# Kernel tuning notes

Hardware: AMD Instinct MI355X
Metric: run time of the kernel (lower is better)

## Reference

```python
import jax, jax.numpy as jnp
import numpy as np

B, S, D = 1, 2048, 2048
HQ, HKV = 32, 8
HD = D // HQ            # 64
G = HQ // HKV           # 4 query heads per kv head


def setup_inputs() -> dict:
    key = jax.random.key(0)
    ks = jax.random.split(key, 5)
    x = jax.random.normal(ks[0], (B, S, D), jnp.float32)
    # RoPE tables (theta = 10000), shape [S, HD//2]
    inv_freq = 1.0 / (10000.0 ** (np.arange(0, HD, 2, dtype=np.float64) / HD))
    angles = np.outer(np.arange(S, dtype=np.float64), inv_freq)
    freqs_cos = jnp.asarray(np.cos(angles), jnp.float32)
    freqs_sin = jnp.asarray(np.sin(angles), jnp.float32)
    # additive causal mask [1,1,S,S]: 0 on/below diagonal, large negative above
    i = jnp.arange(S)
    causal_mask = jnp.where(i[None, :] <= i[:, None], 0.0, -1e9).astype(jnp.float32)[None, None]
    sc = 1.0 / np.sqrt(D)
    Wq = jax.random.normal(ks[1], (D, HQ * HD), jnp.float32) * sc
    Wk = jax.random.normal(ks[2], (D, HKV * HD), jnp.float32) * sc
    Wv = jax.random.normal(ks[3], (D, HKV * HD), jnp.float32) * sc
    Wo = jax.random.normal(ks[4], (D, D), jnp.float32) * sc
    return {"x": x, "freqs_cos": freqs_cos, "freqs_sin": freqs_sin,
            "causal_mask": causal_mask, "Wq": Wq, "Wk": Wk, "Wv": Wv, "Wo": Wo}


def _rope(t, cos, sin):
    # t: [B,S,H,HD]; complex multiply on interleaved (even, odd) pairs
    b, s, h, d = t.shape
    t2 = t.reshape(b, s, h, d // 2, 2)
    t0, t1 = t2[..., 0], t2[..., 1]
    c = cos[None, :, None, :]
    sn = sin[None, :, None, :]
    out = jnp.stack([t0 * c - t1 * sn, t0 * sn + t1 * c], axis=-1)
    return out.reshape(b, s, h, d)


def reference(x, freqs_cos, freqs_sin, causal_mask, Wq, Wk, Wv, Wo):
    b, s, _ = x.shape
    q = (x @ Wq).reshape(b, s, HQ, HD)
    k = (x @ Wk).reshape(b, s, HKV, HD)
    v = (x @ Wv).reshape(b, s, HKV, HD)
    q = _rope(q, freqs_cos, freqs_sin)
    k = _rope(k, freqs_cos, freqs_sin)
    # GQA without materializing repeat_kv: group query heads per kv head
    q = q.transpose(0, 2, 1, 3).reshape(b, HKV, G, s, HD)   # [b,kv,g,s,d]
    k = k.transpose(0, 2, 1, 3)                              # [b,kv,s,d]
    v = v.transpose(0, 2, 1, 3)                              # [b,kv,s,d]
    scores = jnp.einsum('bkgsd,bktd->bkgst', q, k) / jnp.sqrt(jnp.float32(HD))
    scores = scores + causal_mask[:, :, None]                # [1,1,1,S,S] broadcast
    probs = jax.nn.softmax(scores, axis=-1)
    out = jnp.einsum('bkgst,bktd->bkgsd', probs, v)          # [b,kv,g,s,d]
    out = out.transpose(0, 3, 1, 2, 4).reshape(b, s, D)      # merge heads in (kv,g) order
    return out @ Wo
```

## Files before the change

kernel.cpp:

```cpp
#include <hip/hip_runtime.h>

#define SEQ 2048
#define DMODEL 2048

typedef __attribute__((ext_vector_type(8))) _Float16 half8;
typedef __attribute__((ext_vector_type(4))) float f32x4;
typedef __attribute__((ext_vector_type(16))) float f32x16;

typedef const __attribute__((address_space(1))) void* gptr_t;
typedef __attribute__((address_space(3))) void* lptr_t;

static __device__ __forceinline__ void gload16(const void* g, void* l) {
  __builtin_amdgcn_global_load_lds((gptr_t)g, (lptr_t)l, 16, 0, 0);
}

static __device__ __forceinline__ unsigned short f2h(float f) {
  _Float16 h = (_Float16)f;
  union { _Float16 h; unsigned short u; } v; v.h = h;
  return v.u;
}

static __device__ __forceinline__ unsigned int pkh2(float a, float b) {
  union { __fp16 __attribute__((ext_vector_type(2))) h; unsigned int u; } v;
  v.h = __builtin_amdgcn_cvt_pkrtz(a, b);
  return v.u;
}

__global__ void k_cvt(const float* __restrict__ in, unsigned short* __restrict__ out, int n) {
  int i = (blockIdx.x * 256 + threadIdx.x) * 4;
  if (i >= n) return;
  float4 v = *(const float4*)(in + i);
  ushort4 o;
  o.x = f2h(v.x); o.y = f2h(v.y); o.z = f2h(v.z); o.w = f2h(v.w);
  *(ushort4*)(out + i) = o;
}

__global__ void k_tcvt(const float* __restrict__ in, unsigned short* __restrict__ out,
                       int K, int N, int ldin) {
  __shared__ float tile[32][33];
  int n0 = blockIdx.x * 32, k0 = blockIdx.y * 32;
  int tx = threadIdx.x, ty = threadIdx.y;
  #pragma unroll
  for (int j = ty; j < 32; j += 8)
    tile[j][tx] = in[(long)(k0 + j) * ldin + n0 + tx];
  __syncthreads();
  #pragma unroll
  for (int j = ty; j < 32; j += 8)
    out[(long)(n0 + j) * K + k0 + tx] = f2h(tile[tx][j]);
}

__global__ void k_tvp(const unsigned short* __restrict__ in, unsigned short* __restrict__ out) {
  __shared__ unsigned short tile[32][33];
  int c0 = blockIdx.x * 32, s0 = blockIdx.y * 32;
  int tx = threadIdx.x, ty = threadIdx.y;
  #pragma unroll
  for (int j = ty; j < 32; j += 8)
    tile[j][tx] = in[(long)(s0 + j) * 512 + c0 + tx];
  __syncthreads();
  #pragma unroll
  for (int j = ty; j < 32; j += 8) {
    int c = c0 + j;
    int s = s0 + tx;
    int sp = (s & ~12) | ((s & 8) >> 1) | ((s & 4) << 1);
    out[((long)(c >> 6) * 64 + (c & 63)) * SEQ + sp] = tile[tx][j];
  }
}

static __device__ __forceinline__ bool gemm_core(const unsigned short* __restrict__ A,
                                                 const unsigned short* __restrict__ B,
                                                 int K, char* SM, long m0, long n0,
                                                 int& wmO, int& wnO, f32x4 acc[4][4]) {
  int t = threadIdx.x;
  int l = t & 63, w = t >> 6;
  int ks = w & 1, wm = (w >> 2) & 1, wn = (w >> 1) & 1;
  int lr = l & 15, lh = l >> 4;
  wmO = wm; wnO = wn;
  unsigned short* As = (unsigned short*)SM;
  unsigned short* Bs = (unsigned short*)(SM + 32768);

  const unsigned short* Ag = A + (m0 + (t >> 3)) * K + (((t & 7) ^ ((t >> 3) & 7)) * 8);
  const unsigned short* Bg = B + (n0 + (t >> 3)) * K + (((t & 7) ^ ((t >> 3) & 7)) * 8);

  #pragma unroll
  for (int i = 0; i < 4; i++)
    #pragma unroll
    for (int j = 0; j < 4; j++)
      acc[i][j] = (f32x4){0.f, 0.f, 0.f, 0.f};

#define STG(buf, k0) do { \
    gload16(Ag + (k0), As + (buf) * 8192 + t * 8); \
    gload16(Ag + 64 * K + (k0), As + (buf) * 8192 + 4096 + t * 8); \
    gload16(Bg + (k0), Bs + (buf) * 8192 + t * 8); \
    gload16(Bg + 64 * K + (k0), Bs + (buf) * 8192 + 4096 + t * 8); \
  } while (0)

  int T = K >> 6;
  STG(0, 0);
  asm volatile("s_waitcnt vmcnt(0)" ::: "memory");
  __builtin_amdgcn_s_barrier();

  for (int ph = 0; ph < T; ph++) {
    if (ph + 1 < T) STG((ph + 1) & 1, (ph + 1) * 64);
    const unsigned short* Ab = As + (ph & 1) * 8192;
    const unsigned short* Bb = Bs + (ph & 1) * 8192;
    half8 a[4], b[4];
    #pragma unroll
    for (int mf = 0; mf < 4; mf++) {
      int ra = wm * 64 + mf * 16 + lr;
      a[mf] = *(const half8*)&Ab[ra * 64 + (((ks * 4 + lh) ^ (ra & 7)) * 8)];
    }
    #pragma unroll
    for (int nf = 0; nf < 4; nf++) {
      int rb = wn * 64 + nf * 16 + lr;
      b[nf] = *(const half8*)&Bb[rb * 64 + (((ks * 4 + lh) ^ (rb & 7)) * 8)];
    }
    #pragma unroll
    for (int mf = 0; mf < 4; mf++)
      #pragma unroll
      for (int nf = 0; nf < 4; nf++)
        acc[mf][nf] = __builtin_amdgcn_mfma_f32_16x16x32_f16(a[mf], b[nf], acc[mf][nf], 0, 0, 0);
    asm volatile("s_waitcnt vmcnt(0)" ::: "memory");
    __builtin_amdgcn_s_barrier();
  }
#undef STG

  __syncthreads();
  float* red = (float*)SM;
  int p = wm * 2 + wn;
  if (ks == 1) {
    #pragma unroll
    for (int mf = 0; mf < 4; mf++)
      #pragma unroll
      for (int nf = 0; nf < 4; nf++)
        *(f32x4*)&red[p * 4096 + l * 64 + (((mf * 4 + nf) ^ (l & 15)) << 2)] = acc[mf][nf];
  }
  __syncthreads();
  if (ks == 0) {
    #pragma unroll
    for (int mf = 0; mf < 4; mf++)
      #pragma unroll
      for (int nf = 0; nf < 4; nf++)
        acc[mf][nf] += *(const f32x4*)&red[p * 4096 + l * 64 + (((mf * 4 + nf) ^ (l & 15)) << 2)];
  }
  return ks == 0;
}

__global__ __launch_bounds__(512) void k_gemm(const unsigned short* __restrict__ A,
                                              const unsigned short* __restrict__ B,
                                              float* __restrict__ C, int M, int N, int K) {
  __shared__ __align__(16) char SM[65536];
  int l = threadIdx.x & 63;
  int lr = l & 15, lh = l >> 4;
  long m0 = (long)blockIdx.y * 128, n0 = (long)blockIdx.x * 128;
  f32x4 acc[4][4];
  int wm, wn;
  bool own = gemm_core(A, B, K, SM, m0, n0, wm, wn, acc);
  if (own) {
    #pragma unroll
    for (int mf = 0; mf < 4; mf++)
      #pragma unroll
      for (int nf = 0; nf < 4; nf++)
        #pragma unroll
        for (int i = 0; i < 4; i++)
          C[(m0 + wm * 64 + mf * 16 + lh * 4 + i) * N + n0 + wn * 64 + nf * 16 + lr] = acc[mf][nf][i];
  }
}

__global__ __launch_bounds__(512) void k_gemm_qkv(const unsigned short* __restrict__ A,
                                                  const unsigned short* __restrict__ B,
                                                  unsigned short* __restrict__ Qr,
                                                  unsigned short* __restrict__ Kr,
                                                  unsigned short* __restrict__ Vr,
                                                  const float* __restrict__ fc,
                                                  const float* __restrict__ fs, int K) {
  __shared__ __align__(16) char SM[65536];
  int l = threadIdx.x & 63;
  int lr = l & 15, lh = l >> 4;
  long m0 = (long)blockIdx.y * 128, n0 = (long)blockIdx.x * 128;
  f32x4 acc[4][4];
  int wm, wn;
  bool own = gemm_core(A, B, K, SM, m0, n0, wm, wn, acc);
  if (!own) return;

  const float SC = 0.125f * 1.44269504f;
  int n0i = (int)n0;
  if (n0i < 2560) {
    bool isQ = n0i < 2048;
    float scl = isQ ? SC : 1.0f;
    #pragma unroll
    for (int mf = 0; mf < 4; mf++)
      #pragma unroll
      for (int i = 0; i < 4; i++) {
        int row = (int)m0 + wm * 64 + mf * 16 + lh * 4 + i;
        const float* fcr = fc + row * 32;
        const float* fsr = fs + row * 32;
        #pragma unroll
        for (int nf = 0; nf < 4; nf++) {
          float v = acc[mf][nf][i];
          float pv = __shfl_xor(v, 1);
          int col = n0i + wn * 64 + nf * 16 + lr;
          int j = (col & 63) >> 1;
          float c_ = fcr[j] * scl, s_ = fsr[j] * scl;
          float o = (lr & 1) ? (pv * s_ + v * c_) : (v * c_ - pv * s_);
          if (isQ) Qr[(long)row * 2048 + col] = f2h(o);
          else {
            int cc = col - 2048;
            Kr[((long)(cc >> 6) * SEQ + row) * 64 + (cc & 63)] = f2h(o);
          }
        }
      }
  } else {
    #pragma unroll
    for (int mf = 0; mf < 4; mf++)
      #pragma unroll
      for (int i = 0; i < 4; i++) {
        int row = (int)m0 + wm * 64 + mf * 16 + lh * 4 + i;
        #pragma unroll
        for (int nf = 0; nf < 4; nf++) {
          int col = n0i + wn * 64 + nf * 16 + lr;
          Vr[(long)row * 512 + (col - 2560)] = f2h(acc[mf][nf][i]);
        }
      }
  }
}

__global__ __launch_bounds__(256) void k_attn(const unsigned short* __restrict__ Qr,
                                              const unsigned short* __restrict__ Kr,
                                              const unsigned short* __restrict__ Vg,
                                              unsigned short* __restrict__ AO) {
  __shared__ unsigned short KT[2][8192];
  __shared__ unsigned short VT[2][8192];
  __shared__ float gbuf[4][32];

  int tt = threadIdx.x;
  int wid = tt >> 6, l = tt & 63;
  int q = l & 31, hs = l >> 5;
  int h = blockIdx.x, hkv = h >> 2;
  int by = (int)gridDim.y - 1 - blockIdx.y;
  int dt = 4 * by + wid;
  int q0 = by * 128 + wid * 32;

  const unsigned short* Kh = Kr + (long)hkv * SEQ * 64;
  const unsigned short* Vh = Vg + (long)hkv * 64 * SEQ;

  int skr = tt >> 3, skc = tt & 7;
  int svr = tt >> 2, svc = tt & 3;
  const unsigned short* Ksrc = Kh + (long)skr * 64 + ((skc * 8) ^ ((skr & 7) << 3));
  const unsigned short* Vsrc = Vh + (long)svr * SEQ + ((svc * 8) ^ ((svr & 3) << 3));

#define ASTAGE(si) do { \
    int buf_ = (si) & 1; \
    _Pragma("unroll") for (int sub_ = 0; sub_ < 4; sub_++) { \
      int t0_ = ((si) * 4 + sub_) * 32; \
      gload16(Ksrc + (long)t0_ * 64, &KT[buf_][sub_ * 2048 + tt * 8]); \
      gload16(Vsrc + t0_, &VT[buf_][sub_ * 2048 + tt * 8]); \
    } \
  } while (0)

  half8 Qf[4];
  #pragma unroll
  for (int d = 0; d < 4; d++)
    Qf[d] = *(const half8*)&Qr[(long)(q0 + q) * 2048 + h * 64 + d * 16 + 8 * hs];

  f32x16 O0, O1;
  #pragma unroll
  for (int r = 0; r < 16; r++) { O0[r] = 0.f; O1[r] = 0.f; }
  float lsum = 0.f;

  ASTAGE(0);
  asm volatile("s_waitcnt vmcnt(0)" ::: "memory");
  __builtin_amdgcn_s_barrier();

  for (int si = 0; si <= by; si++) {
    if (si + 1 <= by) ASTAGE(si + 1);

    int buf = si & 1;
    #pragma unroll
    for (int sub = 0; sub < 4; sub++) {
      int ti = si * 4 + sub;
      if (ti <= dt) {
        const unsigned short* Ks = &KT[buf][sub * 2048];
        const unsigned short* Vs = &VT[buf][sub * 2048];
        half8 Kf[4], Vf[2][2];
        #pragma unroll
        for (int d = 0; d < 4; d++) {
          int e0 = d * 16 + 8 * hs;
          Kf[d] = *(const half8*)&Ks[q * 64 + (e0 ^ ((q & 7) << 3))];
        }
        #pragma unroll
        for (int ks = 0; ks < 2; ks++)
          #pragma unroll
          for (int nf = 0; nf < 2; nf++) {
            int d = q + 32 * nf;
            int e0 = ks * 16 + 8 * hs;
            Vf[ks][nf] = *(const half8*)&Vs[d * 32 + (e0 ^ ((d & 3) << 3))];
          }

        f32x16 S;
        #pragma unroll
        for (int r = 0; r < 16; r++) S[r] = 0.f;
        #pragma unroll
        for (int d = 0; d < 4; d++)
          S = __builtin_amdgcn_mfma_f32_32x32x16_f16(Kf[d], Qf[d], S, 0, 0, 0);

        bool dg = (ti == dt);
        float p[16];
        #pragma unroll
        for (int r = 0; r < 16; r++) {
          float v = S[r];
          if (dg) {
            int key = (r & 3) + 8 * (r >> 2) + 4 * hs;
            if (key > q) v = -1e30f;
          }
          p[r] = __builtin_exp2f(v - 8.0f);
          lsum += p[r];
        }

        union { unsigned int u[4]; half8 hh; } f0, f1;
        #pragma unroll
        for (int c = 0; c < 4; c++) {
          f0.u[c] = pkh2(p[2 * c], p[2 * c + 1]);
          f1.u[c] = pkh2(p[8 + 2 * c], p[9 + 2 * c]);
        }

        O0 = __builtin_amdgcn_mfma_f32_32x32x16_f16(f0.hh, Vf[0][0], O0, 0, 0, 0);
        O0 = __builtin_amdgcn_mfma_f32_32x32x16_f16(f1.hh, Vf[1][0], O0, 0, 0, 0);
        O1 = __builtin_amdgcn_mfma_f32_32x32x16_f16(f0.hh, Vf[0][1], O1, 0, 0, 0);
        O1 = __builtin_amdgcn_mfma_f32_32x32x16_f16(f1.hh, Vf[1][1], O1, 0, 0, 0);
      }
    }

    asm volatile("s_waitcnt vmcnt(0)" ::: "memory");
    __builtin_amdgcn_s_barrier();
  }
#undef ASTAGE

  lsum += __shfl_xor(lsum, 32);
  if (l < 32) gbuf[wid][l] = 1.f / lsum;
  asm volatile("" ::: "memory");
  #pragma unroll
  for (int r = 0; r < 16; r++) {
    int row = (r & 3) + 8 * (r >> 2) + 4 * hs;
    float ri = gbuf[wid][row];
    AO[(long)(q0 + row) * 2048 + h * 64 + q] = f2h(O0[r] * ri);
    AO[(long)(q0 + row) * 2048 + h * 64 + q + 32] = f2h(O1[r] * ri);
  }
}

extern "C" void kernel_launch(void* const* d_in, const int* in_sizes, int n_in,
                              void* d_out, int out_size, void* d_ws, size_t ws_size,
                              hipStream_t stream) {
  const float* x  = (const float*)d_in[0];
  const float* fc = (const float*)d_in[1];
  const float* fs = (const float*)d_in[2];
  const float* Wq = (const float*)d_in[4];
  const float* Wk = (const float*)d_in[5];
  const float* Wv = (const float*)d_in[6];
  const float* Wo = (const float*)d_in[7];
  float* out = (float*)d_out;

  char* ws = (char*)d_ws;
  unsigned short* xb  = (unsigned short*)(ws);
  unsigned short* WT  = (unsigned short*)(ws + (8l  << 20));
  unsigned short* WoT = (unsigned short*)(ws + (20l << 20));
  unsigned short* Qr  = (unsigned short*)(ws + (28l << 20));
  unsigned short* Kr  = (unsigned short*)(ws + (36l << 20));
  unsigned short* Vr  = (unsigned short*)(ws + (38l << 20));
  unsigned short* Vt  = (unsigned short*)(ws + (40l << 20));
  unsigned short* AO  = xb;

  dim3 tb(32, 8);
  k_cvt<<<4096, 256, 0, stream>>>(x, xb, 2048 * 2048);
  k_tcvt<<<dim3(64, 64), tb, 0, stream>>>(Wq, WT, 2048, 2048, 2048);
  k_tcvt<<<dim3(16, 64), tb, 0, stream>>>(Wk, WT + 2048l * 2048, 2048, 512, 512);
  k_tcvt<<<dim3(16, 64), tb, 0, stream>>>(Wv, WT + 2560l * 2048, 2048, 512, 512);
  k_tcvt<<<dim3(64, 64), tb, 0, stream>>>(Wo, WoT, 2048, 2048, 2048);

  k_gemm_qkv<<<dim3(24, 16), 512, 0, stream>>>(xb, WT, Qr, Kr, Vr, fc, fs, 2048);

  k_tvp<<<dim3(16, 64), tb, 0, stream>>>(Vr, Vt);

  k_attn<<<dim3(32, 16), 256, 0, stream>>>(Qr, Kr, Vt, AO);

  k_gemm<<<dim3(16, 16), 512, 0, stream>>>(AO, WoT, out, 2048, 2048, 2048);
}
```

Measured before the change: 156.9 us.

## Re-layout V tiles in LDS and specialize diagonal masking in attention loop

Changes the V staging layout in shared memory so each lane reads contiguous 8-element chunks indexed by (kslice, d), replacing the XOR-swizzled layout, and changes the global-to-LDS load mapping to match. Splits the per-subtile loop into a templated tile function with separate masked and unmasked variants. Full stages now run four unmasked tiles with no per-tile branch, and the diagonal stage runs only the needed tiles before one masked tile. The aim is to cut LDS bank conflicts and branch/select overhead in the inner loop. The cost is more code and possibly different global load coalescing for V.

```diff
diff --git a/kernel.cpp b/kernel.cpp
--- a/kernel.cpp
+++ b/kernel.cpp
@@ -224,6 +224,55 @@
   }
 }
 
+template <bool DG>
+static __device__ __forceinline__ void attn_tile(const unsigned short* __restrict__ Ks,
+                                                 const unsigned short* __restrict__ Vs,
+                                                 int q, int hs, const half8 (&Qf)[4],
+                                                 f32x16& O0, f32x16& O1, float& lsum) {
+  half8 Kf[4], Vf[2][2];
+  #pragma unroll
+  for (int d = 0; d < 4; d++) {
+    int e0 = d * 16 + 8 * hs;
+    Kf[d] = *(const half8*)&Ks[q * 64 + (e0 ^ ((q & 7) << 3))];
+  }
+  #pragma unroll
+  for (int ks = 0; ks < 2; ks++)
+    #pragma unroll
+    for (int nf = 0; nf < 2; nf++)
+      Vf[ks][nf] = *(const half8*)&Vs[(2 * ks + hs) * 512 + (q + 32 * nf) * 8];
+
+  f32x16 S;
+  #pragma unroll
+  for (int r = 0; r < 16; r++) S[r] = 0.f;
+  #pragma unroll
+  for (int d = 0; d < 4; d++)
+    S = __builtin_amdgcn_mfma_f32_32x32x16_f16(Kf[d], Qf[d], S, 0, 0, 0);
+
+  float p[16];
+  #pragma unroll
+  for (int r = 0; r < 16; r++) {
+    float v = S[r];
+    if (DG) {
+      int key = (r & 3) + 8 * (r >> 2) + 4 * hs;
+      if (key > q) v = -1e30f;
+    }
+    p[r] = __builtin_exp2f(v - 8.0f);
+    lsum += p[r];
+  }
+
+  union { unsigned int u[4]; half8 hh; } f0, f1;
+  #pragma unroll
+  for (int c = 0; c < 4; c++) {
+    f0.u[c] = pkh2(p[2 * c], p[2 * c + 1]);
+    f1.u[c] = pkh2(p[8 + 2 * c], p[9 + 2 * c]);
+  }
+
+  O0 = __builtin_amdgcn_mfma_f32_32x32x16_f16(f0.hh, Vf[0][0], O0, 0, 0, 0);
+  O0 = __builtin_amdgcn_mfma_f32_32x32x16_f16(f1.hh, Vf[1][0], O0, 0, 0, 0);
+  O1 = __builtin_amdgcn_mfma_f32_32x32x16_f16(f0.hh, Vf[0][1], O1, 0, 0, 0);
+  O1 = __builtin_amdgcn_mfma_f32_32x32x16_f16(f1.hh, Vf[1][1], O1, 0, 0, 0);
+}
+
 __global__ __launch_bounds__(256) void k_attn(const unsigned short* __restrict__ Qr,
                                               const unsigned short* __restrict__ Kr,
                                               const unsigned short* __restrict__ Vg,
@@ -244,9 +293,8 @@
   const unsigned short* Vh = Vg + (long)hkv * 64 * SEQ;
 
   int skr = tt >> 3, skc = tt & 7;
-  int svr = tt >> 2, svc = tt & 3;
   const unsigned short* Ksrc = Kh + (long)skr * 64 + ((skc * 8) ^ ((skr & 7) << 3));
-  const unsigned short* Vsrc = Vh + (long)svr * SEQ + ((svc * 8) ^ ((svr & 3) << 3));
+  const unsigned short* Vsrc = Vh + (long)(tt & 63) * SEQ + ((tt >> 6) * 8);
 
 #define ASTAGE(si) do { \
     int buf_ = (si) & 1; \
@@ -275,59 +323,18 @@
     if (si + 1 <= by) ASTAGE(si + 1);
 
     int buf = si & 1;
-    #pragma unroll
-    for (int sub = 0; sub < 4; sub++) {
-      int ti = si * 4 + sub;
-      if (ti <= dt) {
-        const unsigned short* Ks = &KT[buf][sub * 2048];
-        const unsigned short* Vs = &VT[buf][sub * 2048];
-        half8 Kf[4], Vf[2][2];
-        #pragma unroll
-        for (int d = 0; d < 4; d++) {
-          int e0 = d * 16 + 8 * hs;
-          Kf[d] = *(const half8*)&Ks[q * 64 + (e0 ^ ((q & 7) << 3))];
-        }
-        #pragma unroll
-        for (int ks = 0; ks < 2; ks++)
-          #pragma unroll
-          for (int nf = 0; nf < 2; nf++) {
-            int d = q + 32 * nf;
-            int e0 = ks * 16 + 8 * hs;
-            Vf[ks][nf] = *(const half8*)&Vs[d * 32 + (e0 ^ ((d & 3) << 3))];
-          }
-
-        f32x16 S;
-        #pragma unroll
-        for (int r = 0; r < 16; r++) S[r] = 0.f;
-        #pragma unroll
-        for (int d = 0; d < 4; d++)
-          S = __builtin_amdgcn_mfma_f32_32x32x16_f16(Kf[d], Qf[d], S, 0, 0, 0);
-
-        bool dg = (ti == dt);
-        float p[16];
-        #pragma unroll
-        for (int r = 0; r < 16; r++) {
-          float v = S[r];
-          if (dg) {
-            int key = (r & 3) + 8 * (r >> 2) + 4 * hs;
-            if (key > q) v = -1e30f;
-          }
-          p[r] = __builtin_exp2f(v - 8.0f);
-          lsum += p[r];
-        }
-
-        union { unsigned int u[4]; half8 hh; } f0, f1;
-        #pragma unroll
-        for (int c = 0; c < 4; c++) {
-          f0.u[c] = pkh2(p[2 * c], p[2 * c + 1]);
-          f1.u[c] = pkh2(p[8 + 2 * c], p[9 + 2 * c]);
-        }
-
-        O0 = __builtin_amdgcn_mfma_f32_32x32x16_f16(f0.hh, Vf[0][0], O0, 0, 0, 0);
-        O0 = __builtin_amdgcn_mfma_f32_32x32x16_f16(f1.hh, Vf[1][0], O0, 0, 0, 0);
-        O1 = __builtin_amdgcn_mfma_f32_32x32x16_f16(f0.hh, Vf[0][1], O1, 0, 0, 0);
-        O1 = __builtin_amdgcn_mfma_f32_32x32x16_f16(f1.hh, Vf[1][1], O1, 0, 0, 0);
-      }
+    const unsigned short* Kb = &KT[buf][0];
+    const unsigned short* Vb = &VT[buf][0];
+    int rem = dt - si * 4 + 1;
+    if (rem > 4) {
+      attn_tile<false>(Kb, Vb, q, hs, Qf, O0, O1, lsum);
+      attn_tile<false>(Kb + 2048, Vb + 2048, q, hs, Qf, O0, O1, lsum);
+      attn_tile<false>(Kb + 4096, Vb + 4096, q, hs, Qf, O0, O1, lsum);
+      attn_tile<false>(Kb + 6144, Vb + 6144, q, hs, Qf, O0, O1, lsum);
+    } else if (rem > 0) {
+      for (int sub = 0; sub < rem - 1; sub++)
+        attn_tile<false>(Kb + sub * 2048, Vb + sub * 2048, q, hs, Qf, O0, O1, lsum);
+      attn_tile<true>(Kb + (rem - 1) * 2048, Vb + (rem - 1) * 2048, q, hs, Qf, O0, O1, lsum);
     }
 
     asm volatile("s_waitcnt vmcnt(0)" ::: "memory");
```

Result: no change. 155.7 us (-0.7%).
